# Kernel optimization log

Measured on AMD Instinct MI355X. Metric: run time of the kernel, lower is better.

Reference implementation:

```python
import jax, jax.numpy as jnp
import numpy as np

BN_EPS = 1e-5

def _bn_relu(x, gamma, beta, mean, var):
    # x: [B, N, C]; BatchNorm1d(N) in eval mode normalizes over dim=1 (N)
    inv = jax.lax.rsqrt(var + BN_EPS)
    scale = (gamma * inv)[None, :, None]
    shift = (beta - mean * gamma * inv)[None, :, None]
    return jax.nn.relu(x * scale + shift)

def _forward(x, q_gamma, q_beta, q_mean, q_var,
             k_gamma, k_beta, k_mean, k_var,
             v_gamma, v_beta, v_mean, v_var,
             Wq, Wk, Wv, Wp):
    B, C, H, W = x.shape
    N = H * W
    E = Wq.shape[0]
    xs = x.reshape(B, C, N).transpose(0, 2, 1)  # [B, N, C]
    # BN+ReLU over spatial axis, then Linear(N->E) on spatial axis per channel -> [B, E, C]
    q = jnp.einsum('bnc,en->bec', _bn_relu(xs, q_gamma, q_beta, q_mean, q_var), Wq)
    k = jnp.einsum('bnc,en->bec', _bn_relu(xs, k_gamma, k_beta, k_mean, k_var), Wk)
    v = jnp.einsum('bnc,en->bec', _bn_relu(xs, v_gamma, v_beta, v_mean, v_var), Wv)
    scores = jnp.einsum('bec,bfc->bef', q, k) / jnp.sqrt(jnp.asarray(E, x.dtype))  # [B, E, E]
    attn = jax.nn.softmax(scores, axis=-1)
    out = jnp.einsum('bef,bfc->bec', attn, v)          # [B, E, C]
    out = jnp.einsum('bec,ne->bcn', out, Wp)            # Linear(E->N) -> [B, C, N]
    return out.reshape(B, C, H, W)

def setup_inputs() -> dict:
    key = jax.random.key(0)
    ks = jax.random.split(key, 20)
    B, C, H, W = 32, 512, 32, 32
    N = H * W  # sp_dim = 1024
    E = 1024   # embed_dim
    d = {'x': jax.random.normal(ks[0], (B, C, H, W), jnp.float32)}
    i = 1
    for p in ('q', 'k', 'v'):
        d[f'{p}_gamma'] = jax.random.uniform(ks[i], (N,), jnp.float32, 0.5, 1.5); i += 1
        d[f'{p}_beta'] = 0.1 * jax.random.normal(ks[i], (N,), jnp.float32); i += 1
        d[f'{p}_mean'] = 0.1 * jax.random.normal(ks[i], (N,), jnp.float32); i += 1
        d[f'{p}_var'] = jax.random.uniform(ks[i], (N,), jnp.float32, 0.5, 1.5); i += 1
    # torch Linear weight layout: [out, in]; scale ~ 1/sqrt(fan_in)
    d['Wq'] = jax.random.normal(ks[i], (E, N), jnp.float32) * (1.0 / np.sqrt(N)); i += 1
    d['Wk'] = jax.random.normal(ks[i], (E, N), jnp.float32) * (1.0 / np.sqrt(N)); i += 1
    d['Wv'] = jax.random.normal(ks[i], (E, N), jnp.float32) * (1.0 / np.sqrt(N)); i += 1
    d['Wp'] = jax.random.normal(ks[i], (N, E), jnp.float32) * (1.0 / np.sqrt(E)); i += 1
    return d

def reference(x, q_gamma, q_beta, q_mean, q_var,
              k_gamma, k_beta, k_mean, k_var,
              v_gamma, v_beta, v_mean, v_var,
              Wq, Wk, Wv, Wp):
    return _forward(x, q_gamma, q_beta, q_mean, q_var,
                    k_gamma, k_beta, k_mean, k_var,
                    v_gamma, v_beta, v_mean, v_var,
                    Wq, Wk, Wv, Wp)
```

## Files before the change

kernel.cpp:

```cpp
#include <hip/hip_runtime.h>
#include <math.h>

#define BN_EPS 1e-5f

namespace {

constexpr int Bb = 32;
constexpr int Cc = 512;
constexpr int Nn = 1024;
constexpr int Ee = 1024;

typedef __attribute__((ext_vector_type(8))) short short8;
typedef __attribute__((ext_vector_type(4))) float f32x4;
typedef __attribute__((ext_vector_type(4))) unsigned short ushort4_t;

struct bfpair { unsigned short h, l; };

__device__ __forceinline__ unsigned short bf16_rne(float v) {
  unsigned u = __builtin_bit_cast(unsigned, v);
  unsigned r = u + 0x7FFFu + ((u >> 16) & 1u);
  return (unsigned short)(r >> 16);
}
__device__ __forceinline__ float bf16_to_f(unsigned short h) {
  unsigned u = ((unsigned)h) << 16;
  return __builtin_bit_cast(float, u);
}
__device__ __forceinline__ bfpair split_bf(float v) {
  bfpair p;
  p.h = bf16_rne(v);
  p.l = bf16_rne(v - bf16_to_f(p.h));
  return p;
}

__device__ __forceinline__ void gll16(const void* g, void* l) {
  __builtin_amdgcn_global_load_lds(
      (const __attribute__((address_space(1))) void*)g,
      (__attribute__((address_space(3))) void*)l, 16, 0, 0);
}

__global__ __launch_bounds__(256) void prep3(
    const float* __restrict__ qg, const float* __restrict__ qb,
    const float* __restrict__ qm, const float* __restrict__ qv,
    const float* __restrict__ kg, const float* __restrict__ kb,
    const float* __restrict__ km, const float* __restrict__ kv,
    const float* __restrict__ vg, const float* __restrict__ vb,
    const float* __restrict__ vm, const float* __restrict__ vv,
    float* __restrict__ hdr) {
  int i = blockIdx.x * blockDim.x + threadIdx.x;
  if (i < 1024) {
    float inv, sc;
    inv = rsqrtf(qv[i] + BN_EPS); sc = qg[i] * inv;
    hdr[i] = sc;          hdr[1024 + i] = qb[i] - qm[i] * sc;
    inv = rsqrtf(kv[i] + BN_EPS); sc = kg[i] * inv;
    hdr[2048 + i] = sc;   hdr[3072 + i] = kb[i] - km[i] * sc;
    inv = rsqrtf(vv[i] + BN_EPS); sc = vg[i] * inv;
    hdr[4096 + i] = sc;   hdr[5120 + i] = vb[i] - vm[i] * sc;
  }
}

__global__ __launch_bounds__(256) void convert_w(
    const float* __restrict__ wsrc, unsigned short* __restrict__ wh,
    unsigned short* __restrict__ wl, long total4) {
  for (long i = (long)blockIdx.x * 256 + threadIdx.x; i < total4; i += (long)gridDim.x * 256) {
    float4 v = ((const float4*)wsrc)[i];
    bfpair p0 = split_bf(v.x), p1 = split_bf(v.y), p2 = split_bf(v.z), p3 = split_bf(v.w);
    ushort4_t hv, lv;
    hv.x = p0.h; hv.y = p1.h; hv.z = p2.h; hv.w = p3.h;
    lv.x = p0.l; lv.y = p1.l; lv.z = p2.l; lv.w = p3.l;
    *(ushort4_t*)&wh[i * 4] = hv;
    *(ushort4_t*)&wl[i * 4] = lv;
  }
}

__global__ __launch_bounds__(256) void convert_y3(
    const float* __restrict__ x, const float* __restrict__ hdr,
    unsigned short* __restrict__ yqh, unsigned short* __restrict__ yql,
    unsigned short* __restrict__ ykh, unsigned short* __restrict__ ykl,
    unsigned short* __restrict__ dout_us, long b0, long total4) {
  const float* sq = hdr;        const float* tq = hdr + 1024;
  const float* sk = hdr + 2048; const float* tk = hdr + 3072;
  const float* sv = hdr + 4096; const float* tv = hdr + 5120;
  for (long i = (long)blockIdx.x * 256 + threadIdx.x; i < total4; i += (long)gridDim.x * 256) {
    float4 v = ((const float4*)x)[i];
    int n4 = (int)(i & 255);
    float4 a, b;
    ushort4_t hv, lv;
    a = ((const float4*)sq)[n4]; b = ((const float4*)tq)[n4];
    {
      bfpair p0 = split_bf(fmaxf(fmaf(v.x, a.x, b.x), 0.f));
      bfpair p1 = split_bf(fmaxf(fmaf(v.y, a.y, b.y), 0.f));
      bfpair p2 = split_bf(fmaxf(fmaf(v.z, a.z, b.z), 0.f));
      bfpair p3 = split_bf(fmaxf(fmaf(v.w, a.w, b.w), 0.f));
      hv.x = p0.h; hv.y = p1.h; hv.z = p2.h; hv.w = p3.h;
      lv.x = p0.l; lv.y = p1.l; lv.z = p2.l; lv.w = p3.l;
      *(ushort4_t*)&yqh[i * 4] = hv; *(ushort4_t*)&yql[i * 4] = lv;
    }
    a = ((const float4*)sk)[n4]; b = ((const float4*)tk)[n4];
    {
      bfpair p0 = split_bf(fmaxf(fmaf(v.x, a.x, b.x), 0.f));
      bfpair p1 = split_bf(fmaxf(fmaf(v.y, a.y, b.y), 0.f));
      bfpair p2 = split_bf(fmaxf(fmaf(v.z, a.z, b.z), 0.f));
      bfpair p3 = split_bf(fmaxf(fmaf(v.w, a.w, b.w), 0.f));
      hv.x = p0.h; hv.y = p1.h; hv.z = p2.h; hv.w = p3.h;
      lv.x = p0.l; lv.y = p1.l; lv.z = p2.l; lv.w = p3.l;
      *(ushort4_t*)&ykh[i * 4] = hv; *(ushort4_t*)&ykl[i * 4] = lv;
    }
    a = ((const float4*)sv)[n4]; b = ((const float4*)tv)[n4];
    {
      bfpair p0 = split_bf(fmaxf(fmaf(v.x, a.x, b.x), 0.f));
      bfpair p1 = split_bf(fmaxf(fmaf(v.y, a.y, b.y), 0.f));
      bfpair p2 = split_bf(fmaxf(fmaf(v.z, a.z, b.z), 0.f));
      bfpair p3 = split_bf(fmaxf(fmaf(v.w, a.w, b.w), 0.f));
      hv.x = p0.h; hv.y = p1.h; hv.z = p2.h; hv.w = p3.h;
      lv.x = p0.l; lv.y = p1.l; lv.z = p2.l; lv.w = p3.l;
      long g = i >> 17;
      long local = i & 131071;
      unsigned short* slot = dout_us + (b0 + g) * 1048576L;
      *(ushort4_t*)&slot[local * 4] = hv;
      *(ushort4_t*)&slot[524288 + local * 4] = lv;
    }
  }
}

template<bool SPLIT, bool MFIRST>
__global__ __launch_bounds__(256, 2) void gemm3p(
    const unsigned short* __restrict__ Ah, const unsigned short* __restrict__ Al,
    long ldA, long bsA,
    const unsigned short* __restrict__ Bh0, const unsigned short* __restrict__ Bl0,
    const unsigned short* __restrict__ Bh1, const unsigned short* __restrict__ Bl1,
    int msel, long ldB, long bsB,
    float* __restrict__ Cf, unsigned short* __restrict__ Chi, unsigned short* __restrict__ Clo,
    long ldC, long bsC, int K, float alpha, int g0, int g1) {
  __shared__ unsigned short sA[2][2][128][32];
  __shared__ unsigned short sB[2][2][128][32];

  const int nb = gridDim.x;
  int f = blockIdx.x;
  if ((nb & 7) == 0) f = (f & 7) * (nb >> 3) + (f >> 3);
  const int i0 = f % g0, i1 = (f / g0) % g1;
  const long zb = f / (g0 * g1);
  const int m0 = (MFIRST ? i0 : i1) * 128;
  const int n0 = (MFIRST ? i1 : i0) * 128;

  const int t = threadIdx.x, lane = t & 63, w = t >> 6;
  const int sr  = lane >> 2;
  const int skc = (((lane & 3) ^ ((lane >> 3) & 3)) * 8);
  const int wr = w >> 1, wc = w & 1;
  const int fr = lane & 15;
  const int kq = ((((lane >> 4) & 3) ^ ((fr >> 1) & 3)) * 8);

  const unsigned short* Bh = (m0 >= msel) ? Bh1 : Bh0;
  const unsigned short* Bl = (m0 >= msel) ? Bl1 : Bl0;

  const unsigned short* a0 = Ah + zb * bsA + (long)(m0 + w * 32 + sr) * ldA + skc;
  const unsigned short* a1 = Al + zb * bsA + (long)(m0 + w * 32 + sr) * ldA + skc;
  const unsigned short* b0 = Bh + zb * bsB + (long)(n0 + w * 32 + sr) * ldB + skc;
  const unsigned short* b1 = Bl + zb * bsB + (long)(n0 + w * 32 + sr) * ldB + skc;
  const long a16 = 16 * ldA, b16 = 16 * ldB;

  auto STAGE = [&](int buf) {
    gll16(a0, &sA[buf][0][w * 32][0]);  gll16(a0 + a16, &sA[buf][0][w * 32 + 16][0]);
    gll16(a1, &sA[buf][1][w * 32][0]);  gll16(a1 + a16, &sA[buf][1][w * 32 + 16][0]);
    gll16(b0, &sB[buf][0][w * 32][0]);  gll16(b0 + b16, &sB[buf][0][w * 32 + 16][0]);
    gll16(b1, &sB[buf][1][w * 32][0]);  gll16(b1 + b16, &sB[buf][1][w * 32 + 16][0]);
    a0 += 32; a1 += 32; b0 += 32; b1 += 32;
  };

  f32x4 acc[4][4] = {};
  const int nt = K >> 5;

  STAGE(0);
  STAGE(1);
  int cur = 0;

  for (int it = 0; it < nt; ++it) {
    if (it + 1 < nt) asm volatile("s_waitcnt vmcnt(8)" ::: "memory");
    else             asm volatile("s_waitcnt vmcnt(0)" ::: "memory");
    asm volatile("s_barrier" ::: "memory");

    short8 ah[4], al[4], bh[4], bl[4];
#pragma unroll
    for (int i = 0; i < 4; ++i) {
      ah[i] = *(const short8*)&sA[cur][0][wr * 64 + i * 16 + fr][kq];
      al[i] = *(const short8*)&sA[cur][1][wr * 64 + i * 16 + fr][kq];
      bh[i] = *(const short8*)&sB[cur][0][wc * 64 + i * 16 + fr][kq];
      bl[i] = *(const short8*)&sB[cur][1][wc * 64 + i * 16 + fr][kq];
    }

    __builtin_amdgcn_s_setprio(1);
#pragma unroll
    for (int i = 0; i < 4; ++i)
#pragma unroll
      for (int j = 0; j < 4; ++j) {
        acc[i][j] = __builtin_amdgcn_mfma_f32_16x16x32_bf16(ah[i], bh[j], acc[i][j], 0, 0, 0);
        acc[i][j] = __builtin_amdgcn_mfma_f32_16x16x32_bf16(ah[i], bl[j], acc[i][j], 0, 0, 0);
        acc[i][j] = __builtin_amdgcn_mfma_f32_16x16x32_bf16(al[i], bh[j], acc[i][j], 0, 0, 0);
      }
    __builtin_amdgcn_s_setprio(0);

    asm volatile("s_waitcnt lgkmcnt(0)" ::: "memory");
    asm volatile("s_barrier" ::: "memory");
    if (it + 2 < nt) STAGE(cur);
    cur ^= 1;
  }

  const int rb = ((lane >> 4) & 3) * 4;
#pragma unroll
  for (int i = 0; i < 4; ++i)
#pragma unroll
    for (int j = 0; j < 4; ++j) {
      long col = n0 + wc * 64 + j * 16 + fr;
#pragma unroll
      for (int v = 0; v < 4; ++v) {
        long row = m0 + wr * 64 + i * 16 + rb + v;
        float val = acc[i][j][v] * alpha;
        long idx = zb * bsC + row * ldC + col;
        if (SPLIT) {
          bfpair p = split_bf(val);
          Chi[idx] = p.h;
          Clo[idx] = p.l;
        } else {
          Cf[idx] = val;
        }
      }
    }
}

__global__ __launch_bounds__(256) void softmax_rows(float* __restrict__ S) {
  long row = blockIdx.x;
  float* p = S + row * 1024;
  int t = threadIdx.x;
  float4 v = *(float4*)(p + 4 * t);
  float mx = fmaxf(fmaxf(v.x, v.y), fmaxf(v.z, v.w));
#pragma unroll
  for (int i = 1; i < 64; i <<= 1) mx = fmaxf(mx, __shfl_xor(mx, i));
  __shared__ float redm[4];
  __shared__ float reds[4];
  int wave = t >> 6, lane = t & 63;
  if (lane == 0) redm[wave] = mx;
  __syncthreads();
  mx = fmaxf(fmaxf(redm[0], redm[1]), fmaxf(redm[2], redm[3]));
  float e0 = expf(v.x - mx), e1 = expf(v.y - mx);
  float e2 = expf(v.z - mx), e3 = expf(v.w - mx);
  float sum = (e0 + e1) + (e2 + e3);
#pragma unroll
  for (int i = 1; i < 64; i <<= 1) sum += __shfl_xor(sum, i);
  if (lane == 0) reds[wave] = sum;
  __syncthreads();
  sum = (reds[0] + reds[1]) + (reds[2] + reds[3]);
  float inv = 1.0f / sum;
  bfpair p0 = split_bf(e0 * inv), p1 = split_bf(e1 * inv);
  bfpair p2 = split_bf(e2 * inv), p3 = split_bf(e3 * inv);
  ushort4_t hv, lv;
  hv.x = p0.h; hv.y = p1.h; hv.z = p2.h; hv.w = p3.h;
  lv.x = p0.l; lv.y = p1.l; lv.z = p2.l; lv.w = p3.l;
  unsigned short* ph = (unsigned short*)p;
  *(ushort4_t*)&ph[4 * t] = hv;
  *(ushort4_t*)&ph[1024 + 4 * t] = lv;
}

}

extern "C" void kernel_launch(void* const* d_in, const int* in_sizes, int n_in,
                              void* d_out, int out_size, void* d_ws, size_t ws_size,
                              hipStream_t stream) {
  const float* x  = (const float*)d_in[0];
  const float* qg = (const float*)d_in[1];
  const float* qb = (const float*)d_in[2];
  const float* qm = (const float*)d_in[3];
  const float* qv = (const float*)d_in[4];
  const float* kg = (const float*)d_in[5];
  const float* kb = (const float*)d_in[6];
  const float* km = (const float*)d_in[7];
  const float* kv = (const float*)d_in[8];
  const float* vg = (const float*)d_in[9];
  const float* vb = (const float*)d_in[10];
  const float* vm = (const float*)d_in[11];
  const float* vv = (const float*)d_in[12];
  const float* Wq = (const float*)d_in[13];
  const float* Wk = (const float*)d_in[14];
  const float* Wv = (const float*)d_in[15];
  const float* Wp = (const float*)d_in[16];

  const size_t wFix = 65536 + 16UL * 1024 * 1024;
  const size_t perB = 12UL * 1024 * 1024;
  int G = 32;
  while (G > 1 && wFix + (size_t)G * perB > ws_size) G >>= 1;

  char* ws = (char*)d_ws;
  float* hdr = (float*)ws;

  const long WE = 1024L * 1024;
  unsigned short* WQKh = (unsigned short*)(ws + 65536);
  unsigned short* WQKl = WQKh + 2 * WE;
  unsigned short* Wvh  = WQKl + 2 * WE;
  unsigned short* Wvl  = Wvh + WE;
  unsigned short* Wph  = Wvl + WE;
  unsigned short* Wpl  = Wph + WE;

  const long YB = 524288;
  unsigned short* yqh = Wpl + WE;
  unsigned short* yql = yqh + (long)G * YB;
  unsigned short* ykh = yql + (long)G * YB;
  unsigned short* ykl = ykh + (long)G * YB;
  const long QKBS = 1048576;
  unsigned short* QKh = ykl + (long)G * YB;
  unsigned short* QKl = QKh + (long)G * QKBS;
  float* S = (float*)(QKl + (long)G * QKBS);

  unsigned short* dout_us = (unsigned short*)d_out;

  dim3 blk(256);
  const int BIG = 1 << 30;

  prep3<<<dim3(4), blk, 0, stream>>>(qg, qb, qm, qv, kg, kb, km, kv, vg, vb, vm, vv, hdr);

  const long W4 = WE / 4;
  convert_w<<<dim3(1024), blk, 0, stream>>>(Wq, WQKh, WQKl, W4);
  convert_w<<<dim3(1024), blk, 0, stream>>>(Wk, WQKh + WE, WQKl + WE, W4);
  convert_w<<<dim3(1024), blk, 0, stream>>>(Wv, Wvh, Wvl, W4);
  convert_w<<<dim3(1024), blk, 0, stream>>>(Wp, Wph, Wpl, W4);

  for (int b0 = 0; b0 < Bb; b0 += G) {
    const float* xg = x + (size_t)b0 * Cc * Nn;

    convert_y3<<<dim3(2048), blk, 0, stream>>>(
        xg, hdr, yqh, yql, ykh, ykl, dout_us, b0, (long)G * 131072);

    gemm3p<true, true><<<dim3(16 * 4 * G), blk, 0, stream>>>(
        WQKh, WQKl, Nn, 0L,
        yqh, yql, ykh, ykl, 1024, Nn, YB,
        nullptr, QKh, QKl, Cc, QKBS, Nn, 1.0f, 16, 4);

    gemm3p<false, false><<<dim3(8 * 8 * G), blk, 0, stream>>>(
        QKh, QKl, Cc, QKBS,
        QKh + 524288, QKl + 524288, nullptr, nullptr, BIG, Cc, QKBS,
        S, nullptr, nullptr, Ee, 1048576L, Cc, 0.03125f, 8, 8);

    softmax_rows<<<dim3(G * Ee), blk, 0, stream>>>(S);

    gemm3p<true, false><<<dim3(8 * 4 * G), blk, 0, stream>>>(
        dout_us + (long)b0 * 1048576, dout_us + (long)b0 * 1048576 + 524288, Nn, 1048576L,
        Wvh, Wvl, nullptr, nullptr, BIG, Nn, 0L,
        nullptr, yqh, yql, Ee, YB, Nn, 1.0f, 8, 4);

    gemm3p<true, false><<<dim3(8 * 4 * G), blk, 0, stream>>>(
        yqh, yql, Ee, YB,
        (unsigned short*)S, (unsigned short*)S + 1024, nullptr, nullptr, BIG,
        2L * Ee, 2097152L,
        nullptr, QKh, QKl, Ee, QKBS, Ee, 1.0f, 8, 4);

    gemm3p<false, false><<<dim3(8 * 4 * G), blk, 0, stream>>>(
        QKh, QKl, Ee, QKBS,
        Wph, Wpl, nullptr, nullptr, BIG, Ee, 0L,
        (float*)d_out + (size_t)b0 * Cc * Nn, nullptr, nullptr,
        Nn, (long)Cc * Nn, Ee, 1.0f, 8, 4);
  }
}
```

Baseline: 756.9 us.

## Enlarge GEMM tiles to 256x256 and 128x256 with 512-thread blocks

The split-bf16 GEMM kernel now uses 512-thread blocks with 8 waves in a 2x4 layout, and the tile grows to 256 columns with 128 or 256 rows selected by a template parameter. For the 256-row variant, each k-step's compute is split into two halves, and the next stage's global loads are issued between them so they overlap the second half of the MFMAs. Larger tiles raise reuse of shared-memory operands and cut global traffic per FLOP. The cost is fewer blocks per launch, which risks underfilling the CUs, plus more LDS and register pressure (up to 8x4 accumulators) that may limit occupancy.

After: 731.4 us. 1.03x faster.

```diff
diff --git a/kernel.cpp b/kernel.cpp
--- a/kernel.cpp
+++ b/kernel.cpp
@@ -122,8 +122,8 @@
   }
 }
 
-template<bool SPLIT, bool MFIRST>
-__global__ __launch_bounds__(256, 2) void gemm3p(
+template<bool SPLIT, bool MFIRST, int BM>
+__global__ __launch_bounds__(512, 2) void gemm3p(
     const unsigned short* __restrict__ Ah, const unsigned short* __restrict__ Al,
     long ldA, long bsA,
     const unsigned short* __restrict__ Bh0, const unsigned short* __restrict__ Bl0,
@@ -131,42 +131,58 @@
     int msel, long ldB, long bsB,
     float* __restrict__ Cf, unsigned short* __restrict__ Chi, unsigned short* __restrict__ Clo,
     long ldC, long bsC, int K, float alpha, int g0, int g1) {
-  __shared__ unsigned short sA[2][2][128][32];
-  __shared__ unsigned short sB[2][2][128][32];
+  constexpr int WH = BM / 2;
+  constexpr int AF = WH / 16;
+  __shared__ unsigned short sA[2][2][BM][32];
+  __shared__ unsigned short sB[2][2][256][32];
 
   const int nb = gridDim.x;
   int f = blockIdx.x;
   if ((nb & 7) == 0) f = (f & 7) * (nb >> 3) + (f >> 3);
   const int i0 = f % g0, i1 = (f / g0) % g1;
   const long zb = f / (g0 * g1);
-  const int m0 = (MFIRST ? i0 : i1) * 128;
-  const int n0 = (MFIRST ? i1 : i0) * 128;
+  const int m0 = (MFIRST ? i0 : i1) * BM;
+  const int n0 = (MFIRST ? i1 : i0) * 256;
 
   const int t = threadIdx.x, lane = t & 63, w = t >> 6;
+  const int wr = w >> 2, wc = w & 3;
   const int sr  = lane >> 2;
   const int skc = (((lane & 3) ^ ((lane >> 3) & 3)) * 8);
-  const int wr = w >> 1, wc = w & 1;
   const int fr = lane & 15;
   const int kq = ((((lane >> 4) & 3) ^ ((fr >> 1) & 3)) * 8);
 
   const unsigned short* Bh = (m0 >= msel) ? Bh1 : Bh0;
   const unsigned short* Bl = (m0 >= msel) ? Bl1 : Bl0;
 
-  const unsigned short* a0 = Ah + zb * bsA + (long)(m0 + w * 32 + sr) * ldA + skc;
-  const unsigned short* a1 = Al + zb * bsA + (long)(m0 + w * 32 + sr) * ldA + skc;
+  const int aw = w & 3, ahl = w >> 2;
+  const unsigned short* a0;
+  const unsigned short* a1 = nullptr;
+  if (BM == 256) {
+    a0 = Ah + zb * bsA + (long)(m0 + w * 32 + sr) * ldA + skc;
+    a1 = Al + zb * bsA + (long)(m0 + w * 32 + sr) * ldA + skc;
+  } else {
+    a0 = (ahl ? Al : Ah) + zb * bsA + (long)(m0 + aw * 32 + sr) * ldA + skc;
+  }
   const unsigned short* b0 = Bh + zb * bsB + (long)(n0 + w * 32 + sr) * ldB + skc;
   const unsigned short* b1 = Bl + zb * bsB + (long)(n0 + w * 32 + sr) * ldB + skc;
   const long a16 = 16 * ldA, b16 = 16 * ldB;
 
   auto STAGE = [&](int buf) {
-    gll16(a0, &sA[buf][0][w * 32][0]);  gll16(a0 + a16, &sA[buf][0][w * 32 + 16][0]);
-    gll16(a1, &sA[buf][1][w * 32][0]);  gll16(a1 + a16, &sA[buf][1][w * 32 + 16][0]);
+    if constexpr (BM == 256) {
+      gll16(a0, &sA[buf][0][w * 32][0]);  gll16(a0 + a16, &sA[buf][0][w * 32 + 16][0]);
+      gll16(a1, &sA[buf][1][w * 32][0]);  gll16(a1 + a16, &sA[buf][1][w * 32 + 16][0]);
+      a0 += 32; a1 += 32;
+    } else {
+      gll16(a0, &sA[buf][ahl][aw * 32][0]);
+      gll16(a0 + a16, &sA[buf][ahl][aw * 32 + 16][0]);
+      a0 += 32;
+    }
     gll16(b0, &sB[buf][0][w * 32][0]);  gll16(b0 + b16, &sB[buf][0][w * 32 + 16][0]);
     gll16(b1, &sB[buf][1][w * 32][0]);  gll16(b1 + b16, &sB[buf][1][w * 32 + 16][0]);
-    a0 += 32; a1 += 32; b0 += 32; b1 += 32;
+    b0 += 32; b1 += 32;
   };
 
-  f32x4 acc[4][4] = {};
+  f32x4 acc[AF][4] = {};
   const int nt = K >> 5;
 
   STAGE(0);
@@ -174,45 +190,82 @@
   int cur = 0;
 
   for (int it = 0; it < nt; ++it) {
-    if (it + 1 < nt) asm volatile("s_waitcnt vmcnt(8)" ::: "memory");
-    else             asm volatile("s_waitcnt vmcnt(0)" ::: "memory");
+    if (it + 1 < nt) {
+      if constexpr (BM == 256) asm volatile("s_waitcnt vmcnt(8)" ::: "memory");
+      else                     asm volatile("s_waitcnt vmcnt(6)" ::: "memory");
+    } else {
+      asm volatile("s_waitcnt vmcnt(0)" ::: "memory");
+    }
     asm volatile("s_barrier" ::: "memory");
 
-    short8 ah[4], al[4], bh[4], bl[4];
+    short8 bh[4], bl[4], ah[4], al[4];
+#pragma unroll
+    for (int j = 0; j < 4; ++j) {
+      bh[j] = *(const short8*)&sB[cur][0][wc * 64 + j * 16 + fr][kq];
+      bl[j] = *(const short8*)&sB[cur][1][wc * 64 + j * 16 + fr][kq];
+    }
 #pragma unroll
     for (int i = 0; i < 4; ++i) {
-      ah[i] = *(const short8*)&sA[cur][0][wr * 64 + i * 16 + fr][kq];
-      al[i] = *(const short8*)&sA[cur][1][wr * 64 + i * 16 + fr][kq];
-      bh[i] = *(const short8*)&sB[cur][0][wc * 64 + i * 16 + fr][kq];
-      bl[i] = *(const short8*)&sB[cur][1][wc * 64 + i * 16 + fr][kq];
-    }
-
-    __builtin_amdgcn_s_setprio(1);
-#pragma unroll
-    for (int i = 0; i < 4; ++i)
-#pragma unroll
-      for (int j = 0; j < 4; ++j) {
-        acc[i][j] = __builtin_amdgcn_mfma_f32_16x16x32_bf16(ah[i], bh[j], acc[i][j], 0, 0, 0);
-        acc[i][j] = __builtin_amdgcn_mfma_f32_16x16x32_bf16(ah[i], bl[j], acc[i][j], 0, 0, 0);
-        acc[i][j] = __builtin_amdgcn_mfma_f32_16x16x32_bf16(al[i], bh[j], acc[i][j], 0, 0, 0);
+      ah[i] = *(const short8*)&sA[cur][0][wr * WH + i * 16 + fr][kq];
+      al[i] = *(const short8*)&sA[cur][1][wr * WH + i * 16 + fr][kq];
+    }
+
+    if constexpr (BM == 256) {
+      __builtin_amdgcn_s_setprio(1);
+#pragma unroll
+      for (int i = 0; i < 4; ++i)
+#pragma unroll
+        for (int j = 0; j < 4; ++j) {
+          acc[i][j] = __builtin_amdgcn_mfma_f32_16x16x32_bf16(ah[i], bh[j], acc[i][j], 0, 0, 0);
+          acc[i][j] = __builtin_amdgcn_mfma_f32_16x16x32_bf16(ah[i], bl[j], acc[i][j], 0, 0, 0);
+          acc[i][j] = __builtin_amdgcn_mfma_f32_16x16x32_bf16(al[i], bh[j], acc[i][j], 0, 0, 0);
+        }
+      __builtin_amdgcn_s_setprio(0);
+#pragma unroll
+      for (int i = 0; i < 4; ++i) {
+        ah[i] = *(const short8*)&sA[cur][0][wr * WH + (i + 4) * 16 + fr][kq];
+        al[i] = *(const short8*)&sA[cur][1][wr * WH + (i + 4) * 16 + fr][kq];
       }
-    __builtin_amdgcn_s_setprio(0);
-
-    asm volatile("s_waitcnt lgkmcnt(0)" ::: "memory");
-    asm volatile("s_barrier" ::: "memory");
-    if (it + 2 < nt) STAGE(cur);
+      asm volatile("s_waitcnt lgkmcnt(0)" ::: "memory");
+      asm volatile("s_barrier" ::: "memory");
+      if (it + 2 < nt) STAGE(cur);
+      __builtin_amdgcn_s_setprio(1);
+#pragma unroll
+      for (int i = 0; i < 4; ++i)
+#pragma unroll
+        for (int j = 0; j < 4; ++j) {
+          acc[i + 4][j] = __builtin_amdgcn_mfma_f32_16x16x32_bf16(ah[i], bh[j], acc[i + 4][j], 0, 0, 0);
+          acc[i + 4][j] = __builtin_amdgcn_mfma_f32_16x16x32_bf16(ah[i], bl[j], acc[i + 4][j], 0, 0, 0);
+          acc[i + 4][j] = __builtin_amdgcn_mfma_f32_16x16x32_bf16(al[i], bh[j], acc[i + 4][j], 0, 0, 0);
+        }
+      __builtin_amdgcn_s_setprio(0);
+    } else {
+      asm volatile("s_waitcnt lgkmcnt(0)" ::: "memory");
+      asm volatile("s_barrier" ::: "memory");
+      if (it + 2 < nt) STAGE(cur);
+      __builtin_amdgcn_s_setprio(1);
+#pragma unroll
+      for (int i = 0; i < 4; ++i)
+#pragma unroll
+        for (int j = 0; j < 4; ++j) {
+          acc[i][j] = __builtin_amdgcn_mfma_f32_16x16x32_bf16(ah[i], bh[j], acc[i][j], 0, 0, 0);
+          acc[i][j] = __builtin_amdgcn_mfma_f32_16x16x32_bf16(ah[i], bl[j], acc[i][j], 0, 0, 0);
+          acc[i][j] = __builtin_amdgcn_mfma_f32_16x16x32_bf16(al[i], bh[j], acc[i][j], 0, 0, 0);
+        }
+      __builtin_amdgcn_s_setprio(0);
+    }
     cur ^= 1;
   }
 
   const int rb = ((lane >> 4) & 3) * 4;
 #pragma unroll
-  for (int i = 0; i < 4; ++i)
+  for (int i = 0; i < AF; ++i)
 #pragma unroll
     for (int j = 0; j < 4; ++j) {
       long col = n0 + wc * 64 + j * 16 + fr;
 #pragma unroll
       for (int v = 0; v < 4; ++v) {
-        long row = m0 + wr * 64 + i * 16 + rb + v;
+        long row = m0 + wr * WH + i * 16 + rb + v;
         float val = acc[i][j][v] * alpha;
         long idx = zb * bsC + row * ldC + col;
         if (SPLIT) {
@@ -327,33 +380,33 @@
     convert_y3<<<dim3(2048), blk, 0, stream>>>(
         xg, hdr, yqh, yql, ykh, ykl, dout_us, b0, (long)G * 131072);
 
-    gemm3p<true, true><<<dim3(16 * 4 * G), blk, 0, stream>>>(
+    gemm3p<true, true, 256><<<dim3(8 * 2 * G), dim3(512), 0, stream>>>(
         WQKh, WQKl, Nn, 0L,
         yqh, yql, ykh, ykl, 1024, Nn, YB,
-        nullptr, QKh, QKl, Cc, QKBS, Nn, 1.0f, 16, 4);
-
-    gemm3p<false, false><<<dim3(8 * 8 * G), blk, 0, stream>>>(
+        nullptr, QKh, QKl, Cc, QKBS, Nn, 1.0f, 8, 2);
+
+    gemm3p<false, false, 256><<<dim3(4 * 4 * G), dim3(512), 0, stream>>>(
         QKh, QKl, Cc, QKBS,
         QKh + 524288, QKl + 524288, nullptr, nullptr, BIG, Cc, QKBS,
-        S, nullptr, nullptr, Ee, 1048576L, Cc, 0.03125f, 8, 8);
+        S, nullptr, nullptr, Ee, 1048576L, Cc, 0.03125f, 4, 4);
 
     softmax_rows<<<dim3(G * Ee), blk, 0, stream>>>(S);
 
-    gemm3p<true, false><<<dim3(8 * 4 * G), blk, 0, stream>>>(
+    gemm3p<true, false, 128><<<dim3(4 * 4 * G), dim3(512), 0, stream>>>(
         dout_us + (long)b0 * 1048576, dout_us + (long)b0 * 1048576 + 524288, Nn, 1048576L,
         Wvh, Wvl, nullptr, nullptr, BIG, Nn, 0L,
-        nullptr, yqh, yql, Ee, YB, Nn, 1.0f, 8, 4);
-
-    gemm3p<true, false><<<dim3(8 * 4 * G), blk, 0, stream>>>(
+        nullptr, yqh, yql, Ee, YB, Nn, 1.0f, 4, 4);
+
+    gemm3p<true, false, 128><<<dim3(4 * 4 * G), dim3(512), 0, stream>>>(
         yqh, yql, Ee, YB,
         (unsigned short*)S, (unsigned short*)S + 1024, nullptr, nullptr, BIG,
         2L * Ee, 2097152L,
-        nullptr, QKh, QKl, Ee, QKBS, Ee, 1.0f, 8, 4);
-
-    gemm3p<false, false><<<dim3(8 * 4 * G), blk, 0, stream>>>(
+        nullptr, QKh, QKl, Ee, QKBS, Ee, 1.0f, 4, 4);
+
+    gemm3p<false, false, 128><<<dim3(4 * 4 * G), dim3(512), 0, stream>>>(
         QKh, QKl, Ee, QKBS,
         Wph, Wpl, nullptr, nullptr, BIG, Ee, 0L,
         (float*)d_out + (size_t)b0 * Cc * Nn, nullptr, nullptr,
-        Nn, (long)Cc * Nn, Ee, 1.0f, 8, 4);
-  }
-}
+        Nn, (long)Cc * Nn, Ee, 1.0f, 4, 4);
+  }
+}
```
